# Kernel tuning notes

Hardware: AMD Instinct MI355X
Metric: run time of the kernel (lower is better)

Reference implementation:

```python
import jax, jax.numpy as jnp
import numpy as np
import math

B, S, D_IN, D, H, L, NC = 4, 2048, 64, 512, 8, 2, 2
DK = D // H
FACTOR = 5
TOPK = min(FACTOR * int(math.log(S)), S)  # 35
EPS = 1e-5


def make_pe():
    # sinusoidal positional encoding [S, D]
    pos = jnp.arange(S, dtype=jnp.float32)[:, None]
    div = jnp.exp(jnp.arange(0, D, 2, dtype=jnp.float32) * (-math.log(10000.0) / D))
    pe = jnp.zeros((S, D), jnp.float32)
    pe = pe.at[:, 0::2].set(jnp.sin(pos * div)).at[:, 1::2].set(jnp.cos(pos * div))
    return pe


def layernorm(x, g, b):
    m = x.mean(-1, keepdims=True)
    v = x.var(-1, keepdims=True)
    return (x - m) / jnp.sqrt(v + EPS) * g + b


def setup_inputs() -> dict:
    key = jax.random.key(0)
    ks = iter(jax.random.split(key, 16))
    def p(shape, s=0.02):
        return jax.random.normal(next(ks), shape, jnp.float32) * s
    return dict(
        x=jax.random.normal(next(ks), (B, S, D_IN), jnp.float32),
        emb_w=p((D_IN, D)), emb_b=jnp.zeros((D,), jnp.float32),
        wq=p((L, D, D)), bq=jnp.zeros((L, D), jnp.float32),
        wk=p((L, D, D)), bk=jnp.zeros((L, D), jnp.float32),
        wv=p((L, D, D)), bv=jnp.zeros((L, D), jnp.float32),
        wo=p((L, D, D)), bo=jnp.zeros((L, D), jnp.float32),
        ff1_w=p((L, D, 4 * D)), ff1_b=jnp.zeros((L, 4 * D), jnp.float32),
        ff2_w=p((L, 4 * D, D)), ff2_b=jnp.zeros((L, D), jnp.float32),
        ln1_g=jnp.ones((L, D), jnp.float32), ln1_b=jnp.zeros((L, D), jnp.float32),
        ln2_g=jnp.ones((L, D), jnp.float32), ln2_b=jnp.zeros((L, D), jnp.float32),
        dec1_w=p((D, D // 2)), dec1_b=jnp.zeros((D // 2,), jnp.float32),
        dec2_w=p((D // 2, NC)), dec2_b=jnp.zeros((NC,), jnp.float32),
    )


def reference(x, emb_w, emb_b, wq, bq, wk, bk, wv, bv, wo, bo,
              ff1_w, ff1_b, ff2_w, ff2_b, ln1_g, ln1_b, ln2_g, ln2_b,
              dec1_w, dec1_b, dec2_w, dec2_b):
    h = x @ emb_w + emb_b + make_pe()[None]  # [B,S,D]
    scale = 1.0 / math.sqrt(DK)
    for i in range(L):
        q = (h @ wq[i] + bq[i]).reshape(B, S, H, DK).transpose(0, 2, 1, 3)
        k = (h @ wk[i] + bk[i]).reshape(B, S, H, DK).transpose(0, 2, 1, 3)
        v = (h @ wv[i] + bv[i]).reshape(B, S, H, DK).transpose(0, 2, 1, 3)
        scores = jnp.einsum('bhqd,bhkd->bhqk', q, k) * scale  # [B,H,S,S]
        top_scores, _ = jax.lax.top_k(scores, TOPK)            # [B,H,S,TOPK]
        attn = jax.nn.softmax(top_scores, axis=-1)
        # NOTE: faithful to source quirk — V sliced to its FIRST TOPK rows,
        # top_indices are discarded by the original module.
        ao = jnp.einsum('bhqk,bhkd->bhqd', attn, v[:, :, :TOPK, :])
        ao = ao.transpose(0, 2, 1, 3).reshape(B, S, D) @ wo[i] + bo[i]
        h = layernorm(h + ao, ln1_g[i], ln1_b[i])
        ff = jax.nn.relu(h @ ff1_w[i] + ff1_b[i]) @ ff2_w[i] + ff2_b[i]
        h = layernorm(h + ff, ln2_g[i], ln2_b[i])
    pooled = h.mean(axis=1)  # AdaptiveAvgPool1d(1) over seq
    out = jax.nn.relu(pooled @ dec1_w + dec1_b) @ dec2_w + dec2_b  # [B,NC]
    return out
```

## Files before the change

kernel.cpp:

```cpp
#include <hip/hip_runtime.h>
#include <cmath>

typedef unsigned short u16;
typedef __attribute__((ext_vector_type(8))) short short8;
typedef __attribute__((ext_vector_type(4))) float float4v;
typedef unsigned short ushort2v __attribute__((ext_vector_type(2)));

#define S_LEN 2048
#define NTOK  8192
#define TOPK  35
#define NT512 ((size_t)NTOK*512)

__device__ __forceinline__ u16 f2b(float f){
  unsigned int x = __float_as_uint(f);
  unsigned int r = (x + 0x7fffu + ((x >> 16) & 1u)) >> 16;
  return (u16)r;
}
__device__ __forceinline__ float b2f(u16 u){
  return __uint_as_float(((unsigned int)u) << 16);
}

__device__ __forceinline__ unsigned key_of(float f){
  unsigned u = (unsigned)f2b(f);
  unsigned m = (u & 0x8000u) ? 0xFFFFu : 0x8000u;
  return (u ^ m) & 0xFFFFu;
}
__device__ __forceinline__ float key_to_f(unsigned key){
  unsigned m = (key & 0x8000u) ? 0x8000u : 0xFFFFu;
  return __uint_as_float(((key ^ m) & 0xFFFFu) << 16);
}
__device__ __forceinline__ unsigned pkmax(unsigned a, unsigned b){
  union { unsigned u; ushort2v v; } x, y, r;
  x.u = a; y.u = b;
  r.v = __builtin_elementwise_max(x.v, y.v);
  return r.u;
}
__device__ __forceinline__ unsigned pkmin(unsigned a, unsigned b){
  union { unsigned u; ushort2v v; } x, y, r;
  x.u = a; y.u = b;
  r.v = __builtin_elementwise_min(x.v, y.v);
  return r.u;
}

__device__ __forceinline__ void bsort128(unsigned &v0, unsigned &v1, int l){
  #pragma unroll
  for (int k = 2; k <= 128; k <<= 1){
    #pragma unroll
    for (int j = k >> 1; j > 0; j >>= 1){
      if (j == 64){
        unsigned hi = pkmax(v0, v1), lo = pkmin(v0, v1);
        v0 = hi; v1 = lo;
      } else {
        unsigned o0 = (unsigned)__shfl_xor((int)v0, j, 64);
        unsigned o1 = (unsigned)__shfl_xor((int)v1, j, 64);
        bool up0 = (((l & k) == 0) != ((l & j) != 0));
        bool up1 = ((((64 + l) & k) == 0) != ((l & j) != 0));
        unsigned hi0 = pkmax(v0, o0), lo0 = pkmin(v0, o0);
        unsigned hi1 = pkmax(v1, o1), lo1 = pkmin(v1, o1);
        v0 = up0 ? hi0 : lo0;
        v1 = up1 ? hi1 : lo1;
      }
    }
  }
}

__device__ __forceinline__ void gload16(const void* g, void* l){
  __builtin_amdgcn_global_load_lds(
      (const __attribute__((address_space(1))) unsigned int*)g,
      (__attribute__((address_space(3))) unsigned int*)l, 16, 0, 0);
}

struct WtArgs {
  const float* wq; const float* wk; const float* wv; const float* wo;
  const float* ff1w; const float* ff2w;
  u16* wt_qkv; u16* wt_wo; u16* wt_ff1; u16* wt_ff2;
};
__global__ void convert_all(WtArgs a){
  __shared__ u16 t[32][33];
  int l = blockIdx.y;
  int tt = blockIdx.x;
  const float* W; u16* Wt; int K, N, tx_, ty_;
  if (tt < 1024){
    int seg = tt >> 8, r = tt & 255;
    tx_ = r & 15; ty_ = r >> 4; K = 512; N = 512;
    if (seg == 0){ W = a.wq + (size_t)l*262144; Wt = a.wt_qkv + (size_t)l*786432; }
    else if (seg == 1){ W = a.wk + (size_t)l*262144; Wt = a.wt_qkv + (size_t)l*786432 + 262144; }
    else if (seg == 2){ W = a.wv + (size_t)l*262144; Wt = a.wt_qkv + (size_t)l*786432 + 524288; }
    else { W = a.wo + (size_t)l*262144; Wt = a.wt_wo + (size_t)l*262144; }
  } else if (tt < 2048){
    int r = tt - 1024;
    tx_ = r & 63; ty_ = r >> 6; K = 512; N = 2048;
    W = a.ff1w + (size_t)l*1048576; Wt = a.wt_ff1 + (size_t)l*1048576;
  } else {
    int r = tt - 2048;
    tx_ = r & 15; ty_ = r >> 4; K = 2048; N = 512;
    W = a.ff2w + (size_t)l*1048576; Wt = a.wt_ff2 + (size_t)l*1048576;
  }
  int k0 = ty_*32, n0 = tx_*32;
  int tx = threadIdx.x, ty = threadIdx.y;
  #pragma unroll
  for (int i = ty; i < 32; i += 8)
    t[i][tx] = f2b(W[(size_t)(k0+i)*N + n0+tx]);
  __syncthreads();
  #pragma unroll
  for (int i = ty; i < 32; i += 8)
    Wt[(size_t)(n0+i)*K + k0+tx] = t[tx][i];
}

__global__ void embed_kernel(const float* __restrict__ x, const float* __restrict__ w,
                             const float* __restrict__ bias, float* __restrict__ h,
                             u16* __restrict__ h16){
  int t = blockIdx.x;
  int tid = threadIdx.x;
  __shared__ float xs[64];
  if (tid < 64) xs[tid] = x[(size_t)t*64 + tid];
  __syncthreads();
  float acc0 = bias[tid];
  float acc1 = bias[tid + 256];
  #pragma unroll 8
  for (int k = 0; k < 64; ++k){
    float xv = xs[k];
    acc0 += xv * w[k*512 + tid];
    acc1 += xv * w[k*512 + tid + 256];
  }
  int s = t & (S_LEN - 1);
  const float neg_ln1e4_over_D = -9.210340371976184f / 512.f;
  int c0 = tid, c1 = tid + 256;
  float a0 = (float)s * expf((float)(c0 & ~1) * neg_ln1e4_over_D);
  float p0 = (c0 & 1) ? cosf(a0) : sinf(a0);
  float a1 = (float)s * expf((float)(c1 & ~1) * neg_ln1e4_over_D);
  float p1 = (c1 & 1) ? cosf(a1) : sinf(a1);
  float v0 = acc0 + p0, v1 = acc1 + p1;
  h[(size_t)t*512 + c0] = v0;  h16[(size_t)t*512 + c0] = f2b(v0);
  h[(size_t)t*512 + c1] = v1;  h16[(size_t)t*512 + c1] = f2b(v1);
}

template<int EPI>
__global__ __launch_bounds__(256) void gemm_mfma(
    const u16* __restrict__ A, int lda, const u16* __restrict__ Bt, int ldb,
    const float* __restrict__ bias0, const float* __restrict__ bias1,
    const float* __restrict__ bias2,
    float* __restrict__ Cf, u16* __restrict__ C16a, u16* __restrict__ C16b,
    float* __restrict__ Cv, int M, int N, int Klen){
  __shared__ __align__(16) u16 As[128*64];
  __shared__ __align__(16) u16 Bs[128*64];
  int tid = threadIdx.x;
  int w = tid >> 6, l = tid & 63, quad = l >> 4, m = l & 15;
  int gx = gridDim.x;
  int orig = blockIdx.y * gx + blockIdx.x;
  int nwg  = gx * gridDim.y;
  int tt   = (orig & 7) * (nwg >> 3) + (orig >> 3);
  int m0 = (tt / gx) * 128, n0 = (tt % gx) * 128;
  int mh = (w >> 1)*64, nh = (w & 1)*64;
  float4v acc[4][4];
  #pragma unroll
  for (int i = 0; i < 4; ++i)
    #pragma unroll
    for (int j = 0; j < 4; ++j) acc[i][j] = (float4v){0.f,0.f,0.f,0.f};

  for (int kt = 0; kt < Klen; kt += 64){
    #pragma unroll
    for (int c = 0; c < 4; ++c){
      int g = c*256 + tid;
      int row = g >> 3, sc = g & 7, dc = sc ^ (row & 7);
      gload16(A  + (size_t)(m0+row)*lda + kt + dc*8, As + (size_t)g*8);
      gload16(Bt + (size_t)(n0+row)*ldb + kt + dc*8, Bs + (size_t)g*8);
    }
    __syncthreads();
    #pragma unroll
    for (int kk = 0; kk < 2; ++kk){
      short8 af[4], bf[4];
      #pragma unroll
      for (int i = 0; i < 4; ++i){
        int dcx = kk*4 + quad;
        int ra = mh + i*16 + m;
        af[i] = *(const short8*)(As + (size_t)(ra*8 + (dcx ^ (ra & 7)))*8);
        int rb = nh + i*16 + m;
        bf[i] = *(const short8*)(Bs + (size_t)(rb*8 + (dcx ^ (rb & 7)))*8);
      }
      #pragma unroll
      for (int i = 0; i < 4; ++i)
        #pragma unroll
        for (int j = 0; j < 4; ++j)
          acc[i][j] = __builtin_amdgcn_mfma_f32_16x16x32_bf16(af[i], bf[j], acc[i][j], 0, 0, 0);
    }
    __syncthreads();
  }

  #pragma unroll
  for (int i = 0; i < 4; ++i){
    #pragma unroll
    for (int j = 0; j < 4; ++j){
      int col = n0 + nh + j*16 + m;
      #pragma unroll
      for (int r = 0; r < 4; ++r){
        int row = m0 + mh + i*16 + quad*4 + r;
        float v = acc[i][j][r];
        if (EPI == 0){
          Cf[(size_t)row*N + col] = v + bias0[col];
        } else if (EPI == 1){
          C16a[(size_t)row*N + col] = f2b(fmaxf(v + bias0[col], 0.f));
        } else {
          int sel = col >> 9, n5 = col & 511;
          const float* bp = (sel == 0) ? bias0 : (sel == 1) ? bias1 : bias2;
          float vv = v + bp[n5];
          int d = n5 & 63, hh = n5 >> 6;
          int b = row >> 11, s = row & 2047;
          size_t idx = (((size_t)(b*8 + hh))*2048 + s)*64 + d;
          if (sel == 0)      C16a[idx] = f2b(vv);
          else if (sel == 1) C16b[idx] = f2b(vv);
          else               Cv[idx]  = vv;
        }
      }
    }
  }
}

__global__ __launch_bounds__(512, 8) void attn_mfma_topk(
    const u16* __restrict__ qb16, const u16* __restrict__ kb16,
    const float* __restrict__ vb, u16* __restrict__ aob16){
  __shared__ unsigned pr[8*1024];
  int tid  = threadIdx.x;
  int w    = tid >> 6, l = tid & 63;
  int quad = l >> 4,  m = l & 15;
  int orig = blockIdx.y * 128 + blockIdx.x;
  int t4   = ((orig & 7) << 9) | (orig >> 3);
  int bh   = t4 >> 7;
  int q0   = (t4 & 127) << 4;

  const u16* Qp = qb16 + ((size_t)bh*2048 + q0 + m)*64 + quad*8;
  short8 a0 = *(const short8*)Qp;
  short8 a1 = *(const short8*)(Qp + 32);

  const u16* Kbase = kb16 + (size_t)bh*2048*64;
  unsigned sc[32];
  int swz = (quad & 1) << 4;
  const u16* kp0 = Kbase + (size_t)(w*128 + m)*64 + quad*8;
  const uint4* p4 = (const uint4*)(pr + w*1024);

  short8 cb0 = *(const short8*)kp0;
  short8 cb1 = *(const short8*)(kp0 + 32);
  #pragma unroll
  for (int t = 0; t < 16; ++t){
    short8 nb0, nb1;
    if (t < 15){
      int tn = t + 1;
      const u16* np = kp0 + (size_t)(((tn >> 3) << 10) + ((tn & 7) << 4))*64;
      nb0 = *(const short8*)np;
      nb1 = *(const short8*)(np + 32);
    }
    float4v acc = {0.f, 0.f, 0.f, 0.f};
    acc = __builtin_amdgcn_mfma_f32_16x16x32_bf16(a0, cb0, acc, 0, 0, 0);
    acc = __builtin_amdgcn_mfma_f32_16x16x32_bf16(a1, cb1, acc, 0, 0, 0);
    int lk = (w << 7) + ((t & 7) << 4);
    #pragma unroll
    for (int c = 0; c < 2; ++c){
      unsigned lo = key_of(acc[2*c]);
      unsigned hi = key_of(acc[2*c+1]);
      pr[(quad*2 + c)*1024 + ((lk + m) ^ swz)] = lo | (hi << 16);
    }
    cb0 = nb0; cb1 = nb1;
    if (t == 7){
      __syncthreads();
      #pragma unroll
      for (int j = 0; j < 4; ++j){
        uint4 v4 = p4[j*64 + l];
        sc[j*4+0] = v4.x; sc[j*4+1] = v4.y; sc[j*4+2] = v4.z; sc[j*4+3] = v4.w;
      }
      __syncthreads();
    }
  }
  __syncthreads();
  #pragma unroll
  for (int j = 0; j < 4; ++j){
    uint4 v4 = p4[j*64 + l];
    sc[16+j*4+0] = v4.x; sc[16+j*4+1] = v4.y; sc[16+j*4+2] = v4.z; sc[16+j*4+3] = v4.w;
  }

  unsigned* row = &pr[w*1024];

  unsigned m1 = pkmax(sc[0], sc[1]);
  unsigned m2 = pkmin(sc[0], sc[1]);
  #pragma unroll
  for (int i = 2; i < 32; ++i){
    unsigned v = sc[i];
    unsigned nm1 = pkmax(m1, v);
    m2 = pkmax(m2, pkmin(m1, v));
    m1 = nm1;
  }

  unsigned mA1 = m1 & 0xFFFFu, mB1 = m1 >> 16;
  unsigned mA2 = m2 & 0xFFFFu, mB2 = m2 >> 16;
  unsigned tA = 0, tB = 0;
  #pragma unroll
  for (int bit = 15; bit >= 0; --bit){
    unsigned cA = tA | (1u << bit);
    unsigned cB = tB | (1u << bit);
    int nA = __popcll(__ballot(mA1 >= cA)) + __popcll(__ballot(mA2 >= cA));
    int nB = __popcll(__ballot(mB1 >= cB)) + __popcll(__ballot(mB2 >= cB));
    if (nA >= TOPK) tA = cA;
    if (nB >= TOPK) tB = cB;
  }
  unsigned TT = (tA - 1) | ((tB - 1) << 16);

  unsigned mask = 0;
  #pragma unroll
  for (int i = 0; i < 32; ++i){
    mask |= (pkmax(sc[i], TT) != TT) ? (1u << i) : 0u;
  }
  int cnt = __popc(mask);

  int pre = cnt;
  #pragma unroll
  for (int off = 1; off < 64; off <<= 1){
    int n = __shfl_up(pre, off, 64);
    if (l >= off) pre += n;
  }
  pre -= cnt;

  #pragma unroll
  for (int i = 0; i < 32; ++i){
    if (mask & (1u << i)){
      int p = pre + __popc(mask & ((1u << i) - 1u));
      if (p < 128) row[p] = sc[i];
    }
  }
  int tot = __shfl(pre + cnt, 63, 64);

  unsigned c0 = (l < tot)      ? row[l]      : 0u;
  unsigned c1 = (64 + l < tot) ? row[64 + l] : 0u;

  const float* Vb = vb + (size_t)bh*2048*64 + l;
  float vreg[TOPK];
  #pragma unroll
  for (int r = 0; r < TOPK; ++r) vreg[r] = Vb[(size_t)r*64];

  bsort128(c0, c1, l);

  unsigned top0 = (unsigned)__shfl((int)c0, 0, 64);
  float mAf = key_to_f(top0 & 0xFFFFu) * 0.125f;
  float mBf = key_to_f(top0 >> 16)     * 0.125f;
  float tvA = key_to_f(c0 & 0xFFFFu)   * 0.125f;
  float tvB = key_to_f(c0 >> 16)       * 0.125f;
  float wAv = (l < TOPK) ? __expf(tvA - mAf) : 0.f;
  float wBv = (l < TOPK) ? __expf(tvB - mBf) : 0.f;

  float dA = wAv, dB = wBv;
  #pragma unroll
  for (int off = 32; off > 0; off >>= 1){
    dA += __shfl_xor(dA, off, 64);
    dB += __shfl_xor(dB, off, 64);
  }

  float2* wls = (float2*)(row + 128);
  if (l < TOPK) wls[l] = make_float2(wAv, wBv);

  float accA = 0.f, accB = 0.f;
  #pragma unroll
  for (int r = 0; r < TOPK; ++r){
    float2 wv = wls[r];
    float vv = vreg[r];
    accA += wv.x * vv;
    accB += wv.y * vv;
  }
  accA *= __builtin_amdgcn_rcpf(dA);
  accB *= __builtin_amdgcn_rcpf(dB);

  int b = bh >> 3, hh = bh & 7;
  int sA = q0 + w*2;
  aob16[(((size_t)(b*2048 + sA))*8 + hh)*64 + l]     = f2b(accA);
  aob16[(((size_t)(b*2048 + sA + 1))*8 + hh)*64 + l] = f2b(accB);
}

__global__ void resid_ln_kernel(float* __restrict__ h, const float* __restrict__ t,
                                const float* __restrict__ g, const float* __restrict__ b,
                                u16* __restrict__ h16){
  int tok = blockIdx.x;
  int tid = threadIdx.x;
  size_t base2 = (size_t)tok * 256;
  float2 hv = ((const float2*)h)[base2 + tid];
  float2 tv = ((const float2*)t)[base2 + tid];
  float x0 = hv.x + tv.x;
  float x1 = hv.y + tv.y;
  __shared__ float red[8];
  int wid = tid >> 6, lane = tid & 63;

  float s = x0 + x1;
  #pragma unroll
  for (int off = 32; off > 0; off >>= 1) s += __shfl_xor(s, off, 64);
  if (lane == 0) red[wid] = s;
  __syncthreads();
  float mean = (red[0] + red[1] + red[2] + red[3]) * (1.f/512.f);

  float d0 = x0 - mean, d1 = x1 - mean;
  float sq = d0*d0 + d1*d1;
  #pragma unroll
  for (int off = 32; off > 0; off >>= 1) sq += __shfl_xor(sq, off, 64);
  if (lane == 0) red[4 + wid] = sq;
  __syncthreads();
  float var = (red[4] + red[5] + red[6] + red[7]) * (1.f/512.f);
  float inv = rsqrtf(var + 1e-5f);
  float2 gv = ((const float2*)g)[tid];
  float2 bv = ((const float2*)b)[tid];
  float o0 = d0 * inv * gv.x + bv.x;
  float o1 = d1 * inv * gv.y + bv.y;
  ((float2*)h)[base2 + tid] = make_float2(o0, o1);
  ((unsigned*)h16)[base2 + tid] = (unsigned)f2b(o0) | ((unsigned)f2b(o1) << 16);
}

__global__ void pool_zero(float* __restrict__ pooled){
  pooled[blockIdx.x*512 + threadIdx.x] = 0.f;
}
__global__ void pool_kernel(const float* __restrict__ h, float* __restrict__ pooled){
  int c = blockIdx.x * 256 + threadIdx.x;
  int b = blockIdx.y;
  int s0 = blockIdx.z * 64;
  const float* p = h + ((size_t)b * 2048 + s0) * 512 + c;
  float acc = 0.f;
  #pragma unroll 8
  for (int s = 0; s < 64; ++s) acc += p[(size_t)s * 512];
  atomicAdd(&pooled[b*512 + c], acc * (1.f/2048.f));
}

__global__ void decoder_kernel(const float* __restrict__ pooled,
                               const float* __restrict__ w1, const float* __restrict__ b1,
                               const float* __restrict__ w2, const float* __restrict__ b2,
                               float* __restrict__ out){
  __shared__ float ps[4][512];
  __shared__ float hid[4][256];
  int tid = threadIdx.x;
  for (int i = tid; i < 2048; i += 256) ps[i >> 9][i & 511] = pooled[i];
  __syncthreads();
  float bb = b1[tid];
  for (int b = 0; b < 4; ++b){
    float acc = bb;
    for (int k = 0; k < 512; ++k) acc += ps[b][k] * w1[k*256 + tid];
    hid[b][tid] = fmaxf(acc, 0.f);
  }
  __syncthreads();
  if (tid < 8){
    int b = tid >> 1, c = tid & 1;
    float acc = b2[c];
    for (int j = 0; j < 256; ++j) acc += hid[b][j] * w2[j*2 + c];
    out[b*2 + c] = acc;
  }
}

extern "C" void kernel_launch(void* const* d_in, const int* in_sizes, int n_in,
                              void* d_out, int out_size, void* d_ws, size_t ws_size,
                              hipStream_t stream){
  const float* x     = (const float*)d_in[0];
  const float* emb_w = (const float*)d_in[1];
  const float* emb_b = (const float*)d_in[2];
  const float* wq    = (const float*)d_in[3];
  const float* bq    = (const float*)d_in[4];
  const float* wk    = (const float*)d_in[5];
  const float* bk    = (const float*)d_in[6];
  const float* wv    = (const float*)d_in[7];
  const float* bv    = (const float*)d_in[8];
  const float* wo    = (const float*)d_in[9];
  const float* bo    = (const float*)d_in[10];
  const float* ff1w  = (const float*)d_in[11];
  const float* ff1b  = (const float*)d_in[12];
  const float* ff2w  = (const float*)d_in[13];
  const float* ff2b  = (const float*)d_in[14];
  const float* ln1g  = (const float*)d_in[15];
  const float* ln1b  = (const float*)d_in[16];
  const float* ln2g  = (const float*)d_in[17];
  const float* ln2b  = (const float*)d_in[18];
  const float* d1w   = (const float*)d_in[19];
  const float* d1b   = (const float*)d_in[20];
  const float* d2w   = (const float*)d_in[21];
  const float* d2b   = (const float*)d_in[22];

  float* h      = (float*)d_ws;
  float* tmp    = h + NT512;
  u16*   u      = (u16*)(tmp + NT512);
  u16*   h16    = u;
  u16*   q16    = u + NT512;
  u16*   k16    = u + 2*NT512;
  float* vb     = (float*)(u + 3*NT512);
  u16*   ff16   = q16;
  u16*   aob16  = (u16*)(vb + NT512);
  u16*   wt     = aob16 + NT512;
  u16*   wt_qkv = wt;
  u16*   wt_wo  = wt_qkv + (size_t)2*1536*512;
  u16*   wt_ff1 = wt_wo  + (size_t)2*512*512;
  u16*   wt_ff2 = wt_ff1 + (size_t)2*2048*512;
  float* pooled = (float*)(wt_ff2 + (size_t)2*512*2048);

  WtArgs wa{wq, wk, wv, wo, ff1w, ff2w, wt_qkv, wt_wo, wt_ff1, wt_ff2};
  convert_all<<<dim3(3072, 2), dim3(32, 8), 0, stream>>>(wa);

  embed_kernel<<<NTOK, 256, 0, stream>>>(x, emb_w, emb_b, h, h16);

  for (int l = 0; l < 2; ++l){
    gemm_mfma<2><<<dim3(12, 64), 256, 0, stream>>>(
        h16, 512, wt_qkv + (size_t)l*1536*512, 512,
        bq + l*512, bk + l*512, bv + l*512,
        nullptr, q16, k16, vb, NTOK, 1536, 512);

    attn_mfma_topk<<<dim3(128, 32), 512, 0, stream>>>(q16, k16, vb, aob16);

    gemm_mfma<0><<<dim3(4, 64), 256, 0, stream>>>(
        aob16, 512, wt_wo + (size_t)l*512*512, 512,
        bo + l*512, nullptr, nullptr,
        tmp, nullptr, nullptr, nullptr, NTOK, 512, 512);
    resid_ln_kernel<<<NTOK, 256, 0, stream>>>(h, tmp, ln1g + l*512, ln1b + l*512, h16);

    gemm_mfma<1><<<dim3(16, 64), 256, 0, stream>>>(
        h16, 512, wt_ff1 + (size_t)l*2048*512, 512,
        ff1b + l*2048, nullptr, nullptr,
        nullptr, ff16, nullptr, nullptr, NTOK, 2048, 512);

    gemm_mfma<0><<<dim3(4, 64), 256, 0, stream>>>(
        ff16, 2048, wt_ff2 + (size_t)l*512*2048, 2048,
        ff2b + l*512, nullptr, nullptr,
        tmp, nullptr, nullptr, nullptr, NTOK, 512, 2048);
    resid_ln_kernel<<<NTOK, 256, 0, stream>>>(h, tmp, ln2g + l*512, ln2b + l*512, h16);
  }

  pool_zero<<<4, 512, 0, stream>>>(pooled);
  pool_kernel<<<dim3(2, 4, 32), 256, 0, stream>>>(h, pooled);
  decoder_kernel<<<1, 256, 0, stream>>>(pooled, d1w, d1b, d2w, d2b, (float*)d_out);
}
```

Measured before the change: 724.6 us.

## Fuse weight conversion with embedding, vectorize layernorm, drop atomics in pooling

Merges the weight transpose/convert kernel and the embedding kernel into one launch, and the embedding part now handles four tokens per block so each weight row is reused. Layernorm processes two tokens per block with float4 loads. The attention weighted sum reads softmax weights with readlane instead of going through LDS. Pooling writes per-chunk partial sums that the decoder reduces, which removes the zero kernel and the atomics. Together these cut launch count and some memory traffic, at the cost of a larger, branchier prep kernel.

```diff
diff --git a/kernel.cpp b/kernel.cpp
--- a/kernel.cpp
+++ b/kernel.cpp
@@ -75,64 +75,79 @@
   const float* ff1w; const float* ff2w;
   u16* wt_qkv; u16* wt_wo; u16* wt_ff1; u16* wt_ff2;
 };
-__global__ void convert_all(WtArgs a){
+__global__ void prep_kernel(WtArgs a,
+                            const float* __restrict__ x, const float* __restrict__ w,
+                            const float* __restrict__ bias, float* __restrict__ h,
+                            u16* __restrict__ h16){
+  __shared__ float xs[4][64];
   __shared__ u16 t[32][33];
-  int l = blockIdx.y;
-  int tt = blockIdx.x;
-  const float* W; u16* Wt; int K, N, tx_, ty_;
-  if (tt < 1024){
-    int seg = tt >> 8, r = tt & 255;
-    tx_ = r & 15; ty_ = r >> 4; K = 512; N = 512;
-    if (seg == 0){ W = a.wq + (size_t)l*262144; Wt = a.wt_qkv + (size_t)l*786432; }
-    else if (seg == 1){ W = a.wk + (size_t)l*262144; Wt = a.wt_qkv + (size_t)l*786432 + 262144; }
-    else if (seg == 2){ W = a.wv + (size_t)l*262144; Wt = a.wt_qkv + (size_t)l*786432 + 524288; }
-    else { W = a.wo + (size_t)l*262144; Wt = a.wt_wo + (size_t)l*262144; }
-  } else if (tt < 2048){
-    int r = tt - 1024;
-    tx_ = r & 63; ty_ = r >> 6; K = 512; N = 2048;
-    W = a.ff1w + (size_t)l*1048576; Wt = a.wt_ff1 + (size_t)l*1048576;
+  int bx = blockIdx.x;
+  int tid = threadIdx.x;
+  if (bx < 6144){
+    int l  = (bx >= 3072) ? 1 : 0;
+    int tt = bx - l*3072;
+    const float* W; u16* Wt; int K, N, tx_, ty_;
+    if (tt < 1024){
+      int seg = tt >> 8, r = tt & 255;
+      tx_ = r & 15; ty_ = r >> 4; K = 512; N = 512;
+      if (seg == 0){ W = a.wq + (size_t)l*262144; Wt = a.wt_qkv + (size_t)l*786432; }
+      else if (seg == 1){ W = a.wk + (size_t)l*262144; Wt = a.wt_qkv + (size_t)l*786432 + 262144; }
+      else if (seg == 2){ W = a.wv + (size_t)l*262144; Wt = a.wt_qkv + (size_t)l*786432 + 524288; }
+      else { W = a.wo + (size_t)l*262144; Wt = a.wt_wo + (size_t)l*262144; }
+    } else if (tt < 2048){
+      int r = tt - 1024;
+      tx_ = r & 63; ty_ = r >> 6; K = 512; N = 2048;
+      W = a.ff1w + (size_t)l*1048576; Wt = a.wt_ff1 + (size_t)l*1048576;
+    } else {
+      int r = tt - 2048;
+      tx_ = r & 15; ty_ = r >> 4; K = 2048; N = 512;
+      W = a.ff2w + (size_t)l*1048576; Wt = a.wt_ff2 + (size_t)l*1048576;
+    }
+    int k0 = ty_*32, n0 = tx_*32;
+    int tx = tid & 31, ty = tid >> 5;
+    #pragma unroll
+    for (int i = ty; i < 32; i += 8)
+      t[i][tx] = f2b(W[(size_t)(k0+i)*N + n0+tx]);
+    __syncthreads();
+    #pragma unroll
+    for (int i = ty; i < 32; i += 8)
+      Wt[(size_t)(n0+i)*K + k0+tx] = t[tx][i];
   } else {
-    int r = tt - 2048;
-    tx_ = r & 15; ty_ = r >> 4; K = 2048; N = 512;
-    W = a.ff2w + (size_t)l*1048576; Wt = a.wt_ff2 + (size_t)l*1048576;
-  }
-  int k0 = ty_*32, n0 = tx_*32;
-  int tx = threadIdx.x, ty = threadIdx.y;
-  #pragma unroll
-  for (int i = ty; i < 32; i += 8)
-    t[i][tx] = f2b(W[(size_t)(k0+i)*N + n0+tx]);
-  __syncthreads();
-  #pragma unroll
-  for (int i = ty; i < 32; i += 8)
-    Wt[(size_t)(n0+i)*K + k0+tx] = t[tx][i];
-}
-
-__global__ void embed_kernel(const float* __restrict__ x, const float* __restrict__ w,
-                             const float* __restrict__ bias, float* __restrict__ h,
-                             u16* __restrict__ h16){
-  int t = blockIdx.x;
-  int tid = threadIdx.x;
-  __shared__ float xs[64];
-  if (tid < 64) xs[tid] = x[(size_t)t*64 + tid];
-  __syncthreads();
-  float acc0 = bias[tid];
-  float acc1 = bias[tid + 256];
-  #pragma unroll 8
-  for (int k = 0; k < 64; ++k){
-    float xv = xs[k];
-    acc0 += xv * w[k*512 + tid];
-    acc1 += xv * w[k*512 + tid + 256];
-  }
-  int s = t & (S_LEN - 1);
-  const float neg_ln1e4_over_D = -9.210340371976184f / 512.f;
-  int c0 = tid, c1 = tid + 256;
-  float a0 = (float)s * expf((float)(c0 & ~1) * neg_ln1e4_over_D);
-  float p0 = (c0 & 1) ? cosf(a0) : sinf(a0);
-  float a1 = (float)s * expf((float)(c1 & ~1) * neg_ln1e4_over_D);
-  float p1 = (c1 & 1) ? cosf(a1) : sinf(a1);
-  float v0 = acc0 + p0, v1 = acc1 + p1;
-  h[(size_t)t*512 + c0] = v0;  h16[(size_t)t*512 + c0] = f2b(v0);
-  h[(size_t)t*512 + c1] = v1;  h16[(size_t)t*512 + c1] = f2b(v1);
+    int t0 = (bx - 6144) * 4;
+    xs[tid >> 6][tid & 63] = x[(size_t)(t0 + (tid >> 6))*64 + (tid & 63)];
+    __syncthreads();
+    float b0 = bias[tid], b1 = bias[tid + 256];
+    float acc[4][2];
+    #pragma unroll
+    for (int tk = 0; tk < 4; ++tk){ acc[tk][0] = b0; acc[tk][1] = b1; }
+    #pragma unroll 8
+    for (int k = 0; k < 64; ++k){
+      float w0 = w[k*512 + tid];
+      float w1 = w[k*512 + tid + 256];
+      #pragma unroll
+      for (int tk = 0; tk < 4; ++tk){
+        float xv = xs[tk][k];
+        acc[tk][0] += xv * w0;
+        acc[tk][1] += xv * w1;
+      }
+    }
+    const float neg_ln1e4_over_D = -9.210340371976184f / 512.f;
+    int c0 = tid, c1 = tid + 256;
+    float e0 = expf((float)(c0 & ~1) * neg_ln1e4_over_D);
+    float e1 = expf((float)(c1 & ~1) * neg_ln1e4_over_D);
+    #pragma unroll
+    for (int tk = 0; tk < 4; ++tk){
+      int tok = t0 + tk;
+      int s = tok & (S_LEN - 1);
+      float a0 = (float)s * e0;
+      float p0 = (c0 & 1) ? cosf(a0) : sinf(a0);
+      float a1 = (float)s * e1;
+      float p1 = (c1 & 1) ? cosf(a1) : sinf(a1);
+      float v0 = acc[tk][0] + p0, v1 = acc[tk][1] + p1;
+      h[(size_t)tok*512 + c0] = v0;  h16[(size_t)tok*512 + c0] = f2b(v0);
+      h[(size_t)tok*512 + c1] = v1;  h16[(size_t)tok*512 + c1] = f2b(v1);
+    }
+  }
 }
 
 template<int EPI>
@@ -352,16 +367,14 @@
     dB += __shfl_xor(dB, off, 64);
   }
 
-  float2* wls = (float2*)(row + 128);
-  if (l < TOPK) wls[l] = make_float2(wAv, wBv);
-
   float accA = 0.f, accB = 0.f;
   #pragma unroll
   for (int r = 0; r < TOPK; ++r){
-    float2 wv = wls[r];
+    float wA = __uint_as_float((unsigned)__builtin_amdgcn_readlane((int)__float_as_uint(wAv), r));
+    float wB = __uint_as_float((unsigned)__builtin_amdgcn_readlane((int)__float_as_uint(wBv), r));
     float vv = vreg[r];
-    accA += wv.x * vv;
-    accB += wv.y * vv;
+    accA += wA * vv;
+    accB += wB * vv;
   }
   accA *= __builtin_amdgcn_rcpf(dA);
   accB *= __builtin_amdgcn_rcpf(dB);
@@ -375,61 +388,71 @@
 __global__ void resid_ln_kernel(float* __restrict__ h, const float* __restrict__ t,
                                 const float* __restrict__ g, const float* __restrict__ b,
                                 u16* __restrict__ h16){
-  int tok = blockIdx.x;
-  int tid = threadIdx.x;
-  size_t base2 = (size_t)tok * 256;
-  float2 hv = ((const float2*)h)[base2 + tid];
-  float2 tv = ((const float2*)t)[base2 + tid];
-  float x0 = hv.x + tv.x;
-  float x1 = hv.y + tv.y;
+  int half = threadIdx.x >> 7;
+  int tok  = blockIdx.x*2 + half;
+  int tid  = threadIdx.x & 127;
+  size_t base4 = (size_t)tok * 128;
+  float4 hv = ((const float4*)h)[base4 + tid];
+  float4 tv = ((const float4*)t)[base4 + tid];
+  float x0 = hv.x + tv.x, x1 = hv.y + tv.y;
+  float x2 = hv.z + tv.z, x3 = hv.w + tv.w;
   __shared__ float red[8];
-  int wid = tid >> 6, lane = tid & 63;
-
-  float s = x0 + x1;
+  int wid = threadIdx.x >> 6, lane = threadIdx.x & 63;
+
+  float s = (x0 + x1) + (x2 + x3);
   #pragma unroll
   for (int off = 32; off > 0; off >>= 1) s += __shfl_xor(s, off, 64);
   if (lane == 0) red[wid] = s;
   __syncthreads();
-  float mean = (red[0] + red[1] + red[2] + red[3]) * (1.f/512.f);
-
-  float d0 = x0 - mean, d1 = x1 - mean;
-  float sq = d0*d0 + d1*d1;
+  int hb = half << 1;
+  float mean = (red[hb] + red[hb+1]) * (1.f/512.f);
+
+  float d0 = x0 - mean, d1 = x1 - mean, d2 = x2 - mean, d3 = x3 - mean;
+  float sq = (d0*d0 + d1*d1) + (d2*d2 + d3*d3);
   #pragma unroll
   for (int off = 32; off > 0; off >>= 1) sq += __shfl_xor(sq, off, 64);
   if (lane == 0) red[4 + wid] = sq;
   __syncthreads();
-  float var = (red[4] + red[5] + red[6] + red[7]) * (1.f/512.f);
+  float var = (red[4 + hb] + red[4 + hb + 1]) * (1.f/512.f);
   float inv = rsqrtf(var + 1e-5f);
-  float2 gv = ((const float2*)g)[tid];
-  float2 bv = ((const float2*)b)[tid];
+  float4 gv = ((const float4*)g)[tid];
+  float4 bv = ((const float4*)b)[tid];
   float o0 = d0 * inv * gv.x + bv.x;
   float o1 = d1 * inv * gv.y + bv.y;
-  ((float2*)h)[base2 + tid] = make_float2(o0, o1);
-  ((unsigned*)h16)[base2 + tid] = (unsigned)f2b(o0) | ((unsigned)f2b(o1) << 16);
-}
-
-__global__ void pool_zero(float* __restrict__ pooled){
-  pooled[blockIdx.x*512 + threadIdx.x] = 0.f;
-}
-__global__ void pool_kernel(const float* __restrict__ h, float* __restrict__ pooled){
+  float o2 = d2 * inv * gv.z + bv.z;
+  float o3 = d3 * inv * gv.w + bv.w;
+  ((float4*)h)[base4 + tid] = make_float4(o0, o1, o2, o3);
+  uint2 pk;
+  pk.x = (unsigned)f2b(o0) | ((unsigned)f2b(o1) << 16);
+  pk.y = (unsigned)f2b(o2) | ((unsigned)f2b(o3) << 16);
+  ((uint2*)h16)[base4 + tid] = pk;
+}
+
+__global__ void pool_kernel(const float* __restrict__ h, float* __restrict__ part){
   int c = blockIdx.x * 256 + threadIdx.x;
   int b = blockIdx.y;
-  int s0 = blockIdx.z * 64;
-  const float* p = h + ((size_t)b * 2048 + s0) * 512 + c;
+  int z = blockIdx.z;
+  const float* p = h + ((size_t)b * 2048 + z * 64) * 512 + c;
   float acc = 0.f;
   #pragma unroll 8
   for (int s = 0; s < 64; ++s) acc += p[(size_t)s * 512];
-  atomicAdd(&pooled[b*512 + c], acc * (1.f/2048.f));
-}
-
-__global__ void decoder_kernel(const float* __restrict__ pooled,
+  part[((size_t)(z*4 + b))*512 + c] = acc;
+}
+
+__global__ void decoder_kernel(const float* __restrict__ part,
                                const float* __restrict__ w1, const float* __restrict__ b1,
                                const float* __restrict__ w2, const float* __restrict__ b2,
                                float* __restrict__ out){
   __shared__ float ps[4][512];
   __shared__ float hid[4][256];
   int tid = threadIdx.x;
-  for (int i = tid; i < 2048; i += 256) ps[i >> 9][i & 511] = pooled[i];
+  for (int i = tid; i < 2048; i += 256){
+    int b = i >> 9, c = i & 511;
+    float s = 0.f;
+    #pragma unroll
+    for (int z = 0; z < 32; ++z) s += part[((size_t)(z*4 + b))*512 + c];
+    ps[b][c] = s * (1.f/2048.f);
+  }
   __syncthreads();
   float bb = b1[tid];
   for (int b = 0; b < 4; ++b){
@@ -487,12 +510,10 @@
   u16*   wt_wo  = wt_qkv + (size_t)2*1536*512;
   u16*   wt_ff1 = wt_wo  + (size_t)2*512*512;
   u16*   wt_ff2 = wt_ff1 + (size_t)2*2048*512;
-  float* pooled = (float*)(wt_ff2 + (size_t)2*512*2048);
+  float* part   = tmp;
 
   WtArgs wa{wq, wk, wv, wo, ff1w, ff2w, wt_qkv, wt_wo, wt_ff1, wt_ff2};
-  convert_all<<<dim3(3072, 2), dim3(32, 8), 0, stream>>>(wa);
-
-  embed_kernel<<<NTOK, 256, 0, stream>>>(x, emb_w, emb_b, h, h16);
+  prep_kernel<<<8192, 256, 0, stream>>>(wa, x, emb_w, emb_b, h, h16);
 
   for (int l = 0; l < 2; ++l){
     gemm_mfma<2><<<dim3(12, 64), 256, 0, stream>>>(
@@ -506,7 +527,7 @@
         aob16, 512, wt_wo + (size_t)l*512*512, 512,
         bo + l*512, nullptr, nullptr,
         tmp, nullptr, nullptr, nullptr, NTOK, 512, 512);
-    resid_ln_kernel<<<NTOK, 256, 0, stream>>>(h, tmp, ln1g + l*512, ln1b + l*512, h16);
+    resid_ln_kernel<<<NTOK/2, 256, 0, stream>>>(h, tmp, ln1g + l*512, ln1b + l*512, h16);
 
     gemm_mfma<1><<<dim3(16, 64), 256, 0, stream>>>(
         h16, 512, wt_ff1 + (size_t)l*2048*512, 512,
@@ -517,10 +538,9 @@
         ff16, 2048, wt_ff2 + (size_t)l*512*2048, 2048,
         ff2b + l*512, nullptr, nullptr,
         tmp, nullptr, nullptr, nullptr, NTOK, 512, 2048);
-    resid_ln_kernel<<<NTOK, 256, 0, stream>>>(h, tmp, ln2g + l*512, ln2b + l*512, h16);
-  }
-
-  pool_zero<<<4, 512, 0, stream>>>(pooled);
-  pool_kernel<<<dim3(2, 4, 32), 256, 0, stream>>>(h, pooled);
-  decoder_kernel<<<1, 256, 0, stream>>>(pooled, d1w, d1b, d2w, d2b, (float*)d_out);
-}
+    resid_ln_kernel<<<NTOK/2, 256, 0, stream>>>(h, tmp, ln2g + l*512, ln2b + l*512, h16);
+  }
+
+  pool_kernel<<<dim3(2, 4, 32), 256, 0, stream>>>(h, part);
+  decoder_kernel<<<1, 256, 0, stream>>>(part, d1w, d1b, d2w, d2b, (float*)d_out);
+}
```

Result: faster. 709.9 us (-2.0%).
